# Optimization experiments

Measured on AMD Instinct MI355X. Metric: run time of the kernel, lower is better.

The kernel has to match this reference:

```python
import jax, jax.numpy as jnp
import numpy as np

B, T_ENC, T_DEC, D, N_STATE = 32, 1024, 512, 512, 512


def setup_inputs() -> dict:
    key = jax.random.key(0)
    k1, k2, k3, k4 = jax.random.split(key, 4)
    scale = 1.0 / np.sqrt(D)
    return {
        "states_encoder": jax.random.normal(k1, (B, T_ENC, D), dtype=jnp.float32),
        "states_decoder": jax.random.normal(k2, (B, T_DEC, N_STATE), dtype=jnp.float32),
        "Wk": jax.random.normal(k3, (D, N_STATE), dtype=jnp.float32) * scale,
        "bk": jnp.zeros((N_STATE,), dtype=jnp.float32),
        "Wv": jax.random.normal(k4, (D, N_STATE), dtype=jnp.float32) * scale,
        "bv": jnp.zeros((N_STATE,), dtype=jnp.float32),
    }


def reference(states_encoder, states_decoder, Wk, bk, Wv, bv):
    # general Luong dot-product attention (n_state = int branch)
    key_vector = states_encoder @ Wk + bk          # [B, T_enc, N]
    val_vector = states_encoder @ Wv + bv          # [B, T_enc, N]
    # score[b, t_dec, t_enc] = sum_n dec[b,t_dec,n] * key[b,t_enc,n]
    score = jnp.einsum('bqn,bkn->bqk', states_decoder, key_vector)
    attention = jax.nn.softmax(score, axis=-1)     # over encoder positions
    # context[b, t_dec, n] = sum_k attention[b,t_dec,k] * val[b,k,n]
    context = jnp.einsum('bqk,bkn->bqn', attention, val_vector)
    return (context, attention)
```

## Files before the change

kernel.cpp:

```cpp
#include <hip/hip_runtime.h>
#include <math.h>

#define BB    32
#define TENC  1024
#define TDEC  512
#define DDIM  512
#define NST   512

typedef _Float16 f16_t;
typedef _Float16 f16x8 __attribute__((ext_vector_type(8)));
typedef _Float16 f16x4 __attribute__((ext_vector_type(4)));
typedef float    f32x4 __attribute__((ext_vector_type(4)));

#define GLOAD_LDS16(gp, lp) __builtin_amdgcn_global_load_lds( \
    (const __attribute__((address_space(1))) unsigned int*)(const void*)(gp), \
    (__attribute__((address_space(3))) unsigned int*)(lp), 16, 0, 0)

static __device__ __forceinline__ f32x4 MFMA16H(f16x8 a, f16x8 b, f32x4 c) {
    return __builtin_amdgcn_mfma_f32_16x16x32_f16(a, b, c, 0, 0, 0);
}

__global__ __launch_bounds__(256)
void prep_convert(const float* __restrict__ enc, const float* __restrict__ dec,
                  const float* __restrict__ Wk, const float* __restrict__ Wv,
                  f16_t* __restrict__ Ef16, f16_t* __restrict__ dec16,
                  f16_t* __restrict__ Wk16, f16_t* __restrict__ WvT16)
{
    const int bid = blockIdx.x;
    const int t = threadIdx.x;

    if (bid < 12416) {
        const float* src; f16_t* dst; long i;
        if (bid < 8192)       { src = enc; dst = Ef16;  i = (long)bid * 256 + t; }
        else if (bid < 12288) { src = dec; dst = dec16; i = (long)(bid - 8192) * 256 + t; }
        else                  { src = Wk;  dst = Wk16;  i = (long)(bid - 12288) * 256 + t; }
        float4 a = *(const float4*)&src[i * 8];
        float4 b = *(const float4*)&src[i * 8 + 4];
        f16x8 o;
        o[0] = (f16_t)a.x; o[1] = (f16_t)a.y; o[2] = (f16_t)a.z; o[3] = (f16_t)a.w;
        o[4] = (f16_t)b.x; o[5] = (f16_t)b.y; o[6] = (f16_t)b.z; o[7] = (f16_t)b.w;
        *(f16x8*)&dst[i * 8] = o;
        return;
    }

    __shared__ f16_t tile[64][65];
    const int r2 = bid - 12416;
    const int c0 = (r2 & 7) * 64, r0 = (r2 >> 3) * 64;
    const int rr = t >> 4;
    const int cc = (t & 15) * 4;
#pragma unroll
    for (int p = 0; p < 4; ++p) {
        int r = rr + p * 16;
        float4 v = *(const float4*)&Wv[(long)(r0 + r) * NST + c0 + cc];
        tile[r][cc + 0] = (f16_t)v.x;
        tile[r][cc + 1] = (f16_t)v.y;
        tile[r][cc + 2] = (f16_t)v.z;
        tile[r][cc + 3] = (f16_t)v.w;
    }
    __syncthreads();
    const int dr = t >> 2;
    const int tc = (t & 3) * 16;
    f16_t tmp[16];
#pragma unroll
    for (int e = 0; e < 16; ++e) tmp[e] = tile[tc + e][dr];
    *(f16x8*)&WvT16[(long)(c0 + dr) * DDIM + r0 + tc]     = *(f16x8*)&tmp[0];
    *(f16x8*)&WvT16[(long)(c0 + dr) * DDIM + r0 + tc + 8] = *(f16x8*)&tmp[8];
}

template<int EPI>
__global__ __launch_bounds__(256)
void gemm_h(const f16_t* __restrict__ A, const f16_t* __restrict__ B,
            const float* __restrict__ bias, void* __restrict__ C0,
            int M, int N, int K, long sA, long sB, long sC)
{
    __shared__ f16_t lds[2][8192];

    const int tid  = threadIdx.x;
    const int wave = tid >> 6;
    const int lane = tid & 63;

    const int gx = gridDim.x, gy = gridDim.y;
    const long nwg = (long)gx * gy * gridDim.z;
    const long fo  = ((long)blockIdx.z * gy + blockIdx.y) * gx + blockIdx.x;
    const long f2 = (fo & 7) * (nwg >> 3) + (fo >> 3);
    const int bx  = (int)(f2 % gx);
    const int by  = (int)((f2 / gx) % gy);
    const long bz = f2 / ((long)gx * gy);

    const f16_t* Ab = A + bz * sA;
    const f16_t* Bb = B + bz * sB;

    const int row0 = by * 128;
    const int col0 = bx * 128;

    const int srow  = wave * 16 + (lane >> 2);
    const int sslot = (lane & 3) ^ ((srow >> 1) & 3);
    const int wdst  = wave * 512;
    const long aOff0 = (long)(row0 + srow) * K + sslot * 8;
    const long aOff1 = (long)(row0 + 64 + srow) * K + sslot * 8;
    const long bOff0 = (long)(col0 + srow) * K + sslot * 8;
    const long bOff1 = (long)(col0 + 64 + srow) * K + sslot * 8;

    const int fr = lane & 15;
    const int q  = lane >> 4;
    const int wr = (wave >> 1) * 64;
    const int wc = (wave & 1) * 64;
    int aro[4], bro[4];
#pragma unroll
    for (int i = 0; i < 4; ++i) {
        const int r = wr + i * 16 + fr;
        aro[i] = r * 32 + ((q ^ ((r >> 1) & 3)) * 8);
    }
#pragma unroll
    for (int j = 0; j < 4; ++j) {
        const int r = wc + j * 16 + fr;
        bro[j] = r * 32 + ((q ^ ((r >> 1) & 3)) * 8);
    }

    f32x4 acc[4][4] = {};
    const int NT = K >> 5;

#define STAGE(buf, kt) do {                                   \
        GLOAD_LDS16(Ab + aOff0 + (kt), &(buf)[wdst]);         \
        GLOAD_LDS16(Ab + aOff1 + (kt), &(buf)[2048 + wdst]);  \
        GLOAD_LDS16(Bb + bOff0 + (kt), &(buf)[4096 + wdst]);  \
        GLOAD_LDS16(Bb + bOff1 + (kt), &(buf)[6144 + wdst]);  \
    } while (0)

    STAGE(lds[0], 0);

    for (int t = 0; t < NT; ++t) {
        const f16_t* cur = lds[t & 1];
        f16_t* nxt = lds[(t & 1) ^ 1];
        const bool pf = (t + 1 < NT);

        __builtin_amdgcn_sched_barrier(0);
        __builtin_amdgcn_s_barrier();
        if (pf) {
            STAGE(nxt, (t + 1) << 5);
            asm volatile("s_waitcnt vmcnt(4)" ::: "memory");
        } else {
            asm volatile("s_waitcnt vmcnt(0)" ::: "memory");
        }
        __builtin_amdgcn_s_barrier();
        __builtin_amdgcn_sched_barrier(0);

        f16x8 aH[4], bH[4];
#pragma unroll
        for (int i = 0; i < 4; ++i) aH[i] = *(const f16x8*)&cur[aro[i]];
#pragma unroll
        for (int j = 0; j < 4; ++j) bH[j] = *(const f16x8*)&cur[4096 + bro[j]];

#pragma unroll
        for (int j = 0; j < 4; ++j)
#pragma unroll
            for (int i = 0; i < 4; ++i)
                acc[i][j] = MFMA16H(aH[i], bH[j], acc[i][j]);
    }
#undef STAGE

    const int frow = q * 4;
#pragma unroll
    for (int i = 0; i < 4; ++i) {
        const int rgl = row0 + wr + i * 16 + frow;
#pragma unroll
        for (int j = 0; j < 4; ++j) {
            const int cg = col0 + wc + j * 16 + fr;
            if constexpr (EPI == 2) {
                f16_t* C = (f16_t*)C0 + bz * sC;
#pragma unroll
                for (int r = 0; r < 4; ++r)
                    C[(long)(rgl + r) * N + cg] = (f16_t)acc[i][j][r];
            } else {
                float* C = (float*)C0 + bz * sC;
                const float badd = (EPI == 3) ? bias[cg] : 0.0f;
#pragma unroll
                for (int r = 0; r < 4; ++r)
                    C[(long)(rgl + r) * N + cg] = acc[i][j][r] + badd;
            }
        }
    }
}

__global__ __launch_bounds__(512)
void score_softmax(const f16_t* __restrict__ DK, const f16_t* __restrict__ E,
                   float* __restrict__ attn)
{
    __shared__ f16_t Bs[1024 * 32];
    __shared__ f16_t As[32 * 32];
    __shared__ float smx[8][32];
    __shared__ float sms[8][32];

    const int tid  = threadIdx.x;
    const int wave = tid >> 6;
    const int lane = tid & 63;

    const int fo = blockIdx.y * 16 + blockIdx.x;
    const int f2 = (fo & 7) * 64 + (fo >> 3);
    const int rg = f2 & 15;
    const int z  = f2 >> 4;

    const f16_t* DKb = DK + ((long)z * TDEC + rg * 32) * DDIM;
    const f16_t* Eb  = E + (long)z * TENC * DDIM;
    float* Ab = attn + (long)z * TDEC * TENC + (long)(rg * 32) * TENC;

    const int srow = lane >> 2;
    const int sk   = lane & 3;

    const int fr = lane & 15;
    const int q  = lane >> 4;
    const int wc = wave * 128;
    int aro[2], bro[8];
#pragma unroll
    for (int i = 0; i < 2; ++i) {
        const int r = i * 16 + fr;
        aro[i] = r * 32 + ((q ^ ((r >> 1) & 3)) * 8);
    }
#pragma unroll
    for (int j = 0; j < 8; ++j) {
        const int r = wc + j * 16 + fr;
        bro[j] = r * 32 + ((q ^ ((r >> 1) & 3)) * 8);
    }

    f32x4 acc[2][8] = {};

#define SSTAGE(ktd) do {                                                       \
        _Pragma("unroll")                                                      \
        for (int c = 0; c < 8; ++c) {                                          \
            const int rL = wave * 128 + c * 16 + srow;                         \
            const int slot = sk ^ ((rL >> 1) & 3);                             \
            GLOAD_LDS16(Eb + (long)rL * DDIM + (ktd) + slot * 8,               \
                        &Bs[(wave * 128 + c * 16) * 32]);                      \
        }                                                                      \
        if (wave == 0) {                                                       \
            _Pragma("unroll")                                                  \
            for (int c = 0; c < 2; ++c) {                                      \
                const int rA = c * 16 + srow;                                  \
                const int slot = sk ^ ((rA >> 1) & 3);                         \
                GLOAD_LDS16(DKb + (long)rA * DDIM + (ktd) + slot * 8,          \
                            &As[c * 16 * 32]);                                 \
            }                                                                  \
        }                                                                      \
    } while (0)

    SSTAGE(0);

    for (int kt = 0; kt < 16; ++kt) {
        asm volatile("s_waitcnt vmcnt(0)" ::: "memory");
        __builtin_amdgcn_s_barrier();
        __builtin_amdgcn_sched_barrier(0);

        f16x8 aH[2];
        aH[0] = *(const f16x8*)&As[aro[0]];
        aH[1] = *(const f16x8*)&As[aro[1]];
#pragma unroll
        for (int j = 0; j < 8; ++j) {
            f16x8 bH = *(const f16x8*)&Bs[bro[j]];
            acc[0][j] = MFMA16H(aH[0], bH, acc[0][j]);
            acc[1][j] = MFMA16H(aH[1], bH, acc[1][j]);
        }
        asm volatile("s_waitcnt lgkmcnt(0)" ::: "memory");
        __builtin_amdgcn_sched_barrier(0);
        __builtin_amdgcn_s_barrier();
        if (kt < 15) SSTAGE((kt + 1) * 32);
    }
#undef SSTAGE

    float pm[2][4];
#pragma unroll
    for (int i = 0; i < 2; ++i)
#pragma unroll
        for (int rr = 0; rr < 4; ++rr) {
            float m = acc[i][0][rr];
#pragma unroll
            for (int j = 1; j < 8; ++j) m = fmaxf(m, acc[i][j][rr]);
            pm[i][rr] = m;
        }
#pragma unroll
    for (int o = 1; o < 16; o <<= 1)
#pragma unroll
        for (int i = 0; i < 2; ++i)
#pragma unroll
            for (int rr = 0; rr < 4; ++rr)
                pm[i][rr] = fmaxf(pm[i][rr], __shfl_xor(pm[i][rr], o, 16));
    if (fr == 0) {
#pragma unroll
        for (int i = 0; i < 2; ++i)
#pragma unroll
            for (int rr = 0; rr < 4; ++rr)
                smx[wave][i * 16 + q * 4 + rr] = pm[i][rr];
    }
    __syncthreads();
    float gm[2][4];
#pragma unroll
    for (int i = 0; i < 2; ++i)
#pragma unroll
        for (int rr = 0; rr < 4; ++rr) {
            const int row = i * 16 + q * 4 + rr;
            float m = smx[0][row];
#pragma unroll
            for (int w = 1; w < 8; ++w) m = fmaxf(m, smx[w][row]);
            gm[i][rr] = m;
        }
    float ps[2][4] = {};
#pragma unroll
    for (int i = 0; i < 2; ++i)
#pragma unroll
        for (int j = 0; j < 8; ++j)
#pragma unroll
            for (int rr = 0; rr < 4; ++rr) {
                float e = __expf(acc[i][j][rr] - gm[i][rr]);
                acc[i][j][rr] = e;
                ps[i][rr] += e;
            }
#pragma unroll
    for (int o = 1; o < 16; o <<= 1)
#pragma unroll
        for (int i = 0; i < 2; ++i)
#pragma unroll
            for (int rr = 0; rr < 4; ++rr)
                ps[i][rr] += __shfl_xor(ps[i][rr], o, 16);
    if (fr == 0) {
#pragma unroll
        for (int i = 0; i < 2; ++i)
#pragma unroll
            for (int rr = 0; rr < 4; ++rr)
                sms[wave][i * 16 + q * 4 + rr] = ps[i][rr];
    }
    __syncthreads();
#pragma unroll
    for (int i = 0; i < 2; ++i)
#pragma unroll
        for (int rr = 0; rr < 4; ++rr) {
            const int row = i * 16 + q * 4 + rr;
            float s = sms[0][row];
#pragma unroll
            for (int w = 1; w < 8; ++w) s += sms[w][row];
            const float inv = 1.0f / s;
#pragma unroll
            for (int j = 0; j < 8; ++j)
                Ab[(long)row * TENC + wc + j * 16 + fr] = acc[i][j][rr] * inv;
        }
}

__global__ __launch_bounds__(256)
void gemm_ctx(const float* __restrict__ Af, const f16_t* __restrict__ Bh,
              const float* __restrict__ bias, float* __restrict__ C,
              int M, int N, int K, long sAf, long sB, long sC)
{
    __shared__ f16_t lds[2][8192];

    const int tid  = threadIdx.x;
    const int wave = tid >> 6;
    const int lane = tid & 63;

    const int gx = gridDim.x, gy = gridDim.y;
    const long nwg = (long)gx * gy * gridDim.z;
    const long fo  = ((long)blockIdx.z * gy + blockIdx.y) * gx + blockIdx.x;
    const long f2 = (fo & 7) * (nwg >> 3) + (fo >> 3);
    const int bx  = (int)(f2 % gx);
    const int by  = (int)((f2 / gx) % gy);
    const long bz = f2 / ((long)gx * gy);

    const float* AfB = Af + bz * sAf;
    const f16_t* BhB = Bh + bz * sB;

    const int row0 = by * 128;
    const int col0 = bx * 128;

    const int srow  = wave * 16 + (lane >> 2);
    const int sslot = (lane & 3) ^ ((srow >> 1) & 3);
    const int wdst  = wave * 512;

    const int rrow = tid >> 3;
    const int rk4  = (tid & 7) * 4;
    const int rgr  = rk4 >> 3;
    const int rh4  = rk4 & 4;

    const int fr = lane & 15;
    const int q  = lane >> 4;
    const int wr = (wave >> 1) * 64;
    const int wc = (wave & 1) * 64;
    int aro[4], bro[4];
#pragma unroll
    for (int i = 0; i < 4; ++i) {
        const int r = wr + i * 16 + fr;
        aro[i] = r * 32 + ((q ^ ((r >> 1) & 3)) * 8);
    }
#pragma unroll
    for (int j = 0; j < 4; ++j) {
        const int r = wc + j * 16 + fr;
        bro[j] = r * 32 + ((q ^ ((r >> 1) & 3)) * 8);
    }

    f32x4 acc[4][4] = {};
    float4 rS[4];
    f16x8 aH[4], bH[4];
    const int NT = K >> 5;

    auto stageG = [&](f16_t* buf, int kt) {
#pragma unroll
        for (int c = 0; c < 2; ++c) {
            const long go = (long)(col0 + c * 64 + srow) * K + kt + sslot * 8;
            GLOAD_LDS16(BhB + go, &buf[4096 + c * 2048 + wdst]);
        }
    };
    auto loadR = [&](int kt) {
#pragma unroll
        for (int i = 0; i < 4; ++i)
            rS[i] = *(const float4*)&AfB[(long)(row0 + i * 32 + rrow) * K + kt + rk4];
    };
    auto writeR = [&](f16_t* buf) {
#pragma unroll
        for (int i = 0; i < 4; ++i) {
            const int row = i * 32 + rrow;
            const int eo  = row * 32 + ((rgr ^ ((row >> 1) & 3)) * 8) + rh4;
            f16x4 h4;
            h4[0] = (f16_t)rS[i].x; h4[1] = (f16_t)rS[i].y;
            h4[2] = (f16_t)rS[i].z; h4[3] = (f16_t)rS[i].w;
            *(f16x4*)&buf[eo] = h4;
        }
    };
    auto readF = [&](const f16_t* buf) {
#pragma unroll
        for (int i = 0; i < 4; ++i) aH[i] = *(const f16x8*)&buf[aro[i]];
#pragma unroll
        for (int j = 0; j < 4; ++j) bH[j] = *(const f16x8*)&buf[4096 + bro[j]];
    };

    loadR(0);
    stageG(lds[0], 0);
    writeR(lds[0]);
    loadR(32);
    asm volatile("s_waitcnt vmcnt(4)" ::: "memory");
    asm volatile("s_waitcnt lgkmcnt(0)" ::: "memory");
    __builtin_amdgcn_s_barrier();
    readF(lds[0]);
    asm volatile("s_waitcnt lgkmcnt(0)" ::: "memory");
    __builtin_amdgcn_s_barrier();

    for (int t = 0; t < NT; ++t) {
        f16_t* nxt = lds[(t & 1) ^ 1];
        const bool pf = (t + 1 < NT);

        if (pf) {
            writeR(nxt);
            stageG(nxt, (t + 1) << 5);
            if (t + 2 < NT) loadR((t + 2) << 5);
        }
#pragma unroll
        for (int j = 0; j < 4; ++j)
#pragma unroll
            for (int i = 0; i < 4; ++i)
                acc[i][j] = MFMA16H(aH[i], bH[j], acc[i][j]);

        if (pf && (t + 2 < NT))
            asm volatile("s_waitcnt vmcnt(4)" ::: "memory");
        else
            asm volatile("s_waitcnt vmcnt(0)" ::: "memory");
        asm volatile("s_waitcnt lgkmcnt(0)" ::: "memory");
        __builtin_amdgcn_s_barrier();
        if (pf) {
            readF(nxt);
            asm volatile("s_waitcnt lgkmcnt(0)" ::: "memory");
        }
        __builtin_amdgcn_s_barrier();
    }

    const int frow = q * 4;
#pragma unroll
    for (int i = 0; i < 4; ++i) {
        const int rgl = row0 + wr + i * 16 + frow;
#pragma unroll
        for (int j = 0; j < 4; ++j) {
            const int cg = col0 + wc + j * 16 + fr;
            float* Cp = C + bz * sC;
            const float badd = bias[cg];
#pragma unroll
            for (int r = 0; r < 4; ++r)
                Cp[(long)(rgl + r) * N + cg] = acc[i][j][r] + badd;
        }
    }
}

__global__ __launch_bounds__(256)
void softmax_rows(float* __restrict__ S)
{
    const long row = (long)blockIdx.x * 4 + (threadIdx.x >> 6);
    const int lane = threadIdx.x & 63;
    float* p = S + row * (long)TENC;
    float4 v[4];
    float m = -INFINITY;
#pragma unroll
    for (int i = 0; i < 4; ++i) {
        v[i] = *(const float4*)&p[i * 256 + lane * 4];
        m = fmaxf(fmaxf(fmaxf(v[i].x, v[i].y), fmaxf(v[i].z, v[i].w)), m);
    }
#pragma unroll
    for (int o = 32; o; o >>= 1) m = fmaxf(m, __shfl_xor(m, o, 64));
    float s = 0.f;
#pragma unroll
    for (int i = 0; i < 4; ++i) {
        v[i].x = __expf(v[i].x - m); v[i].y = __expf(v[i].y - m);
        v[i].z = __expf(v[i].z - m); v[i].w = __expf(v[i].w - m);
        s += v[i].x + v[i].y + v[i].z + v[i].w;
    }
#pragma unroll
    for (int o = 32; o; o >>= 1) s += __shfl_xor(s, o, 64);
    const float inv = 1.0f / s;
#pragma unroll
    for (int i = 0; i < 4; ++i) {
        v[i].x *= inv; v[i].y *= inv; v[i].z *= inv; v[i].w *= inv;
        *(float4*)&p[i * 256 + lane * 4] = v[i];
    }
}

#define TILE_M 64
#define TILE_N 64
#define TILE_K 16
template<bool B_TRANS, bool ADD_BIAS>
__global__ __launch_bounds__(256)
void gemm_f32(const float* __restrict__ A, const float* __restrict__ Bm,
              const float* __restrict__ bias, float* __restrict__ C,
              int M, int N, int K, int lda, int ldb,
              long strideA, long strideB, long strideC)
{
    __shared__ float As[TILE_K][TILE_M + 4];
    __shared__ float Bs[TILE_K][TILE_N + 4];
    const int b = blockIdx.z;
    A += (long)b * strideA; Bm += (long)b * strideB; C += (long)b * strideC;
    const int tid = threadIdx.x;
    const int tx = tid & 15, ty = tid >> 4;
    const int row0 = blockIdx.y * TILE_M, col0 = blockIdx.x * TILE_N;
    const int am = tid >> 2, ak = (tid & 3) * 4;
    float acc[4][4] = {};
    for (int kt = 0; kt < K; kt += TILE_K) {
        float4 a4 = *(const float4*)&A[(long)(row0 + am) * lda + kt + ak];
        float4 b4;
        if (B_TRANS) b4 = *(const float4*)&Bm[(long)(col0 + am) * ldb + kt + ak];
        else {
            const int bk_ = tid >> 4, bn = (tid & 15) * 4;
            b4 = *(const float4*)&Bm[(long)(kt + bk_) * ldb + col0 + bn];
        }
        __syncthreads();
        As[ak + 0][am] = a4.x; As[ak + 1][am] = a4.y;
        As[ak + 2][am] = a4.z; As[ak + 3][am] = a4.w;
        if (B_TRANS) {
            Bs[ak + 0][am] = b4.x; Bs[ak + 1][am] = b4.y;
            Bs[ak + 2][am] = b4.z; Bs[ak + 3][am] = b4.w;
        } else {
            const int bk_ = tid >> 4, bn = (tid & 15) * 4;
            *(float4*)&Bs[bk_][bn] = b4;
        }
        __syncthreads();
#pragma unroll
        for (int k = 0; k < TILE_K; ++k) {
            float4 av = *(const float4*)&As[k][ty * 4];
            float4 bv4 = *(const float4*)&Bs[k][tx * 4];
            float ar[4] = {av.x, av.y, av.z, av.w};
            float br[4] = {bv4.x, bv4.y, bv4.z, bv4.w};
#pragma unroll
            for (int i = 0; i < 4; ++i)
#pragma unroll
                for (int j = 0; j < 4; ++j)
                    acc[i][j] = fmaf(ar[i], br[j], acc[i][j]);
        }
    }
    float4 bias4 = make_float4(0.f, 0.f, 0.f, 0.f);
    if (ADD_BIAS) bias4 = *(const float4*)&bias[col0 + tx * 4];
#pragma unroll
    for (int i = 0; i < 4; ++i) {
        float4 o;
        o.x = acc[i][0] + bias4.x; o.y = acc[i][1] + bias4.y;
        o.z = acc[i][2] + bias4.z; o.w = acc[i][3] + bias4.w;
        *(float4*)&C[(long)(row0 + ty * 4 + i) * N + col0 + tx * 4] = o;
    }
}

extern "C" void kernel_launch(void* const* d_in, const int* in_sizes, int n_in,
                              void* d_out, int out_size, void* d_ws, size_t ws_size,
                              hipStream_t stream)
{
    const float* enc = (const float*)d_in[0];
    const float* dec = (const float*)d_in[1];
    const float* Wk  = (const float*)d_in[2];
    const float* Wv  = (const float*)d_in[4];
    const float* bv  = (const float*)d_in[5];

    const long nD = (long)BB * TDEC * NST;

    float* ctx   = (float*)d_out;
    float* attnF = ctx + nD;

    const size_t need = 68157440;
    const dim3 blk(256);

    if (ws_size < need) {
        float* ws = (float*)d_ws;
        gemm_f32<true, false><<<dim3(DDIM / 64, (BB * TDEC) / 64, 1), blk, 0, stream>>>(
            dec, Wk, nullptr, ws, BB * TDEC, DDIM, NST, NST, NST, 0, 0, 0);
        gemm_f32<true, false><<<dim3(TENC / 64, TDEC / 64, BB), blk, 0, stream>>>(
            ws, enc, nullptr, attnF, TDEC, TENC, DDIM, DDIM, DDIM,
            (long)TDEC * DDIM, (long)TENC * DDIM, (long)TDEC * TENC);
        softmax_rows<<<(BB * TDEC) / 4, blk, 0, stream>>>(attnF);
        gemm_f32<false, false><<<dim3(DDIM / 64, TDEC / 64, BB), blk, 0, stream>>>(
            attnF, enc, nullptr, ws, TDEC, DDIM, TENC, TENC, DDIM,
            (long)TDEC * TENC, (long)TENC * DDIM, (long)TDEC * DDIM);
        gemm_f32<false, true><<<dim3(NST / 64, (BB * TDEC) / 64, 1), blk, 0, stream>>>(
            ws, Wv, bv, ctx, BB * TDEC, NST, DDIM, DDIM, NST, 0, 0, 0);
        return;
    }

    char* w = (char*)d_ws;
    f16_t* EVT   = (f16_t*)(w);
    f16_t* Ef16  = (f16_t*)(w + 33554432);
    f16_t* Wk16  = (f16_t*)(w + 67108864);
    f16_t* WvT16 = (f16_t*)(w + 67633152);

    f16_t* dec16 = (f16_t*)ctx;
    f16_t* DK16  = dec16 + nD;

    prep_convert<<<12480, blk, 0, stream>>>(enc, dec, Wk, Wv,
                                            Ef16, dec16, Wk16, WvT16);

    gemm_h<2><<<dim3(DDIM / 128, (BB * TDEC) / 128, 1), blk, 0, stream>>>(
        dec16, Wk16, nullptr, DK16,
        BB * TDEC, DDIM, NST, 0, 0, 0);

    gemm_h<2><<<dim3(TENC / 128, NST / 128, BB), blk, 0, stream>>>(
        WvT16, Ef16, nullptr, EVT,
        NST, TENC, DDIM,
        0, (long)TENC * DDIM, (long)NST * TENC);

    score_softmax<<<dim3(16, 32), dim3(512), 0, stream>>>(DK16, Ef16, attnF);

    gemm_ctx<<<dim3(NST / 128, TDEC / 128, BB), blk, 0, stream>>>(
        attnF, EVT, bv, ctx,
        TDEC, NST, TENC,
        (long)TDEC * TENC, (long)NST * TENC, (long)TDEC * NST);
}
```

Before: 160.9 us.

## Double-buffer score_softmax LDS tiles and split encoder columns into two halves

The score+softmax kernel now stages encoder and decoder-key tiles into two alternating LDS buffers, so the next k-tile's global-to-LDS load is issued before the MFMAs on the current tile run. Each buffer holds only 512 encoder rows, so the 1024-column row is processed as two sequential 16-step passes into separate accumulator sets. Partial vmcnt waits let the load overlap compute instead of stalling on a full drain every step. Each workgroup now issues twice as many barrier-separated steps with half the MFMAs per step, which adds sync overhead.

```diff
diff --git a/kernel.cpp b/kernel.cpp
--- a/kernel.cpp
+++ b/kernel.cpp
@@ -186,8 +186,8 @@
 void score_softmax(const f16_t* __restrict__ DK, const f16_t* __restrict__ E,
                    float* __restrict__ attn)
 {
-    __shared__ f16_t Bs[1024 * 32];
-    __shared__ f16_t As[32 * 32];
+    __shared__ f16_t Bs[2][512 * 32];
+    __shared__ f16_t As[2][32 * 32];
     __shared__ float smx[8][32];
     __shared__ float sms[8][32];
 
@@ -209,61 +209,71 @@
 
     const int fr = lane & 15;
     const int q  = lane >> 4;
-    const int wc = wave * 128;
-    int aro[2], bro[8];
+    int aro[2], bro[4];
 #pragma unroll
     for (int i = 0; i < 2; ++i) {
         const int r = i * 16 + fr;
         aro[i] = r * 32 + ((q ^ ((r >> 1) & 3)) * 8);
     }
 #pragma unroll
-    for (int j = 0; j < 8; ++j) {
-        const int r = wc + j * 16 + fr;
+    for (int j = 0; j < 4; ++j) {
+        const int r = wave * 64 + j * 16 + fr;
         bro[j] = r * 32 + ((q ^ ((r >> 1) & 3)) * 8);
     }
 
-    f32x4 acc[2][8] = {};
-
-#define SSTAGE(ktd) do {                                                       \
+    f32x4 acc0[2][4] = {};
+    f32x4 acc1[2][4] = {};
+
+#define SSTAGE(b, h, kt) do {                                                  \
+        f16_t* Bdst = Bs[b];                                                   \
         _Pragma("unroll")                                                      \
-        for (int c = 0; c < 8; ++c) {                                          \
-            const int rL = wave * 128 + c * 16 + srow;                         \
+        for (int c = 0; c < 4; ++c) {                                          \
+            const int rL = wave * 64 + c * 16 + srow;                          \
             const int slot = sk ^ ((rL >> 1) & 3);                             \
-            GLOAD_LDS16(Eb + (long)rL * DDIM + (ktd) + slot * 8,               \
-                        &Bs[(wave * 128 + c * 16) * 32]);                      \
+            GLOAD_LDS16(Eb + ((long)((h) * 512 + rL)) * DDIM + (kt) * 32 + slot * 8, \
+                        &Bdst[(wave * 64 + c * 16) * 32]);                     \
         }                                                                      \
         if (wave == 0) {                                                       \
+            f16_t* Adst = As[b];                                               \
             _Pragma("unroll")                                                  \
             for (int c = 0; c < 2; ++c) {                                      \
                 const int rA = c * 16 + srow;                                  \
                 const int slot = sk ^ ((rA >> 1) & 3);                         \
-                GLOAD_LDS16(DKb + (long)rA * DDIM + (ktd) + slot * 8,          \
-                            &As[c * 16 * 32]);                                 \
+                GLOAD_LDS16(DKb + (long)rA * DDIM + (kt) * 32 + slot * 8,      \
+                            &Adst[c * 16 * 32]);                               \
             }                                                                  \
         }                                                                      \
     } while (0)
 
-    SSTAGE(0);
-
-    for (int kt = 0; kt < 16; ++kt) {
-        asm volatile("s_waitcnt vmcnt(0)" ::: "memory");
-        __builtin_amdgcn_s_barrier();
-        __builtin_amdgcn_sched_barrier(0);
-
-        f16x8 aH[2];
-        aH[0] = *(const f16x8*)&As[aro[0]];
-        aH[1] = *(const f16x8*)&As[aro[1]];
-#pragma unroll
-        for (int j = 0; j < 8; ++j) {
-            f16x8 bH = *(const f16x8*)&Bs[bro[j]];
-            acc[0][j] = MFMA16H(aH[0], bH, acc[0][j]);
-            acc[1][j] = MFMA16H(aH[1], bH, acc[1][j]);
-        }
-        asm volatile("s_waitcnt lgkmcnt(0)" ::: "memory");
-        __builtin_amdgcn_sched_barrier(0);
-        __builtin_amdgcn_s_barrier();
-        if (kt < 15) SSTAGE((kt + 1) * 32);
-    }
+#define KSTEP(ACC, it) do {                                                    \
+        const bool pf = (it) + 1 < 32;                                         \
+        __builtin_amdgcn_sched_barrier(0);                                     \
+        __builtin_amdgcn_s_barrier();                                          \
+        if (pf) {                                                              \
+            SSTAGE(((it) + 1) & 1, ((it) + 1) >> 4, ((it) + 1) & 15);          \
+            if (wave == 0) asm volatile("s_waitcnt vmcnt(6)" ::: "memory");    \
+            else           asm volatile("s_waitcnt vmcnt(4)" ::: "memory");    \
+        } else {                                                               \
+            asm volatile("s_waitcnt vmcnt(0)" ::: "memory");                   \
+        }                                                                      \
+        __builtin_amdgcn_s_barrier();                                          \
+        __builtin_amdgcn_sched_barrier(0);                                     \
+        const f16_t* Acur = As[(it) & 1];                                      \
+        const f16_t* Bcur = Bs[(it) & 1];                                      \
+        f16x8 aH0 = *(const f16x8*)&Acur[aro[0]];                              \
+        f16x8 aH1 = *(const f16x8*)&Acur[aro[1]];                              \
+        _Pragma("unroll")                                                      \
+        for (int j = 0; j < 4; ++j) {                                          \
+            f16x8 bH = *(const f16x8*)&Bcur[bro[j]];                           \
+            ACC[0][j] = MFMA16H(aH0, bH, ACC[0][j]);                           \
+            ACC[1][j] = MFMA16H(aH1, bH, ACC[1][j]);                           \
+        }                                                                      \
+    } while (0)
+
+    SSTAGE(0, 0, 0);
+    for (int kt = 0; kt < 16; ++kt) KSTEP(acc0, kt);
+    for (int kt = 0; kt < 16; ++kt) KSTEP(acc1, 16 + kt);
+#undef KSTEP
 #undef SSTAGE
 
     float pm[2][4];
@@ -271,9 +281,11 @@
     for (int i = 0; i < 2; ++i)
 #pragma unroll
         for (int rr = 0; rr < 4; ++rr) {
-            float m = acc[i][0][rr];
-#pragma unroll
-            for (int j = 1; j < 8; ++j) m = fmaxf(m, acc[i][j][rr]);
+            float m = acc0[i][0][rr];
+#pragma unroll
+            for (int j = 1; j < 4; ++j) m = fmaxf(m, acc0[i][j][rr]);
+#pragma unroll
+            for (int j = 0; j < 4; ++j) m = fmaxf(m, acc1[i][j][rr]);
             pm[i][rr] = m;
         }
 #pragma unroll
@@ -306,12 +318,14 @@
 #pragma unroll
     for (int i = 0; i < 2; ++i)
 #pragma unroll
-        for (int j = 0; j < 8; ++j)
+        for (int j = 0; j < 4; ++j)
 #pragma unroll
             for (int rr = 0; rr < 4; ++rr) {
-                float e = __expf(acc[i][j][rr] - gm[i][rr]);
-                acc[i][j][rr] = e;
-                ps[i][rr] += e;
+                float e0 = __expf(acc0[i][j][rr] - gm[i][rr]);
+                float e1 = __expf(acc1[i][j][rr] - gm[i][rr]);
+                acc0[i][j][rr] = e0;
+                acc1[i][j][rr] = e1;
+                ps[i][rr] += e0 + e1;
             }
 #pragma unroll
     for (int o = 1; o < 16; o <<= 1)
@@ -338,8 +352,10 @@
             for (int w = 1; w < 8; ++w) s += sms[w][row];
             const float inv = 1.0f / s;
 #pragma unroll
-            for (int j = 0; j < 8; ++j)
-                Ab[(long)row * TENC + wc + j * 16 + fr] = acc[i][j][rr] * inv;
+            for (int j = 0; j < 4; ++j) {
+                Ab[(long)row * TENC + wave * 64 + j * 16 + fr]       = acc0[i][j][rr] * inv;
+                Ab[(long)row * TENC + 512 + wave * 64 + j * 16 + fr] = acc1[i][j][rr] * inv;
+            }
         }
 }
 
```

Measured after the change: 157.9 us. No clear change (-1.8%).
